# Kernel optimization log

Measured on AMD Instinct MI355X. Metric: run time of the kernel, lower is better.

The kernel has to match this reference:

```python
import jax, jax.numpy as jnp
import numpy as np


def _fracdiff(X, alpha):
    """Fractional differencing (1-L)^alpha applied per batch/channel.
    X: (B, T, n), alpha: (B, n) >= 0. Weights w_0 = 1, w_k = w_{k-1}*(k-1-alpha)/k.
    Y[b, t, i] = sum_{k=0..t} w[b, k, i] * X[b, t-k, i]  (causal filter).
    Computed as a linear convolution via FFT (same math, O(T log T)).
    """
    B, T, n = X.shape
    k = jnp.arange(1, T, dtype=X.dtype)[None, :, None]          # (1, T-1, 1)
    factors = (k - 1.0 - alpha[:, None, :]) / k                  # (B, T-1, n)
    w = jnp.concatenate(
        [jnp.ones((B, 1, n), X.dtype), jnp.cumprod(factors, axis=1)], axis=1
    )                                                            # (B, T, n)
    L = 2 * T  # zero-pad to avoid circular wrap-around
    Xf = jnp.fft.rfft(X, n=L, axis=1)
    Wf = jnp.fft.rfft(w, n=L, axis=1)
    Y = jnp.fft.irfft(Xf * Wf, n=L, axis=1)[:, :T, :]
    return Y.astype(X.dtype)


def setup_inputs() -> dict:
    key = jax.random.key(0)
    kx, ka, kA = jax.random.split(key, 3)
    B, T, n = 8, 8192, 128
    X = jax.random.normal(kx, (B, T, n), dtype=jnp.float32)
    # normalize per trial/channel, mirroring normalize_data=True in __init__
    X = (X - X.mean(axis=1, keepdims=True)) / X.std(axis=1, keepdims=True, ddof=1)
    alpha = jax.random.uniform(ka, (B, n), dtype=jnp.float32)
    A = jax.random.normal(kA, (B, n, n), dtype=jnp.float32) * 0.1
    return {"X": X, "alpha": alpha, "A": A}


def reference(X, alpha, A):
    # _resid(): Y = fracdiff(X, relu(alpha)); E = Y[:,1:,:] - X[:,:-1,:] @ A^T
    Y = _fracdiff(X, jax.nn.relu(alpha))
    Yhat = jnp.einsum('bti,bji->btj', X[:, :-1, :], A)  # bmm(X, A.transpose(1,2))
    return Y[:, 1:, :] - Yhat
```

## Files before the change

### kernel.cpp

```cpp
#include <hip/hip_runtime.h>

#define T 8192
#define NCH 128
#define NB 8
#define NS (NB * NCH)
#define TM1 (T - 1)

typedef __bf16 v8bf __attribute__((ext_vector_type(8)));
typedef float v16f __attribute__((ext_vector_type(16)));

#define WREV_LEN 8448
#define WREV_COPY_STRIDE ((size_t)NS * WREV_LEN)

#define ILIM_TRUNC 144
#define KCHUNKS 19
#define WR_D_MIN 2880

struct __attribute__((packed, aligned(4))) U16 { uint4 v; };
struct __attribute__((packed, aligned(4))) F16V { float4 v; };

__device__ __forceinline__ uint bf_bits(float f) {
  union { float f; uint u; } v; v.f = f;
  return (v.u + 0x7FFFu + ((v.u >> 16) & 1u)) >> 16;
}

__device__ __forceinline__ uint wbits(const float* wsh, int k) {
  if ((unsigned)k > 8191u) return 0u;
  return bf_bits(wsh[k + (k >> 5)]);
}

__global__ __launch_bounds__(256) void wkern(const float* __restrict__ alpha,
                                             ushort* __restrict__ wr2) {
  const int sid = blockIdx.x;
  const float a = fmaxf(alpha[sid], 0.f);
  const int j = threadIdx.x;
  __shared__ float sc[256];
  __shared__ float wsh[8448];
  const int k0 = j << 5;
  float c = 1.f;
  #pragma unroll
  for (int s = 1; s <= 32; ++s) {
    const float k = (float)(k0 + s);
    c *= (k - 1.f - a) / k;
  }
  sc[j] = c;
  __syncthreads();
  for (int off = 1; off < 256; off <<= 1) {
    const float u = (j >= off) ? sc[j - off] : 1.f;
    const float v = sc[j];
    __syncthreads();
    sc[j] = u * v;
    __syncthreads();
  }
  float p = (j == 0) ? 1.f : sc[j - 1];
  wsh[k0 + j] = p;
  for (int s = 1; s < 32; ++s) {
    const float k = (float)(k0 + s);
    p *= (k - 1.f - a) / k;
    wsh[k0 + s + j] = p;
  }
  __syncthreads();
  uint* c0u = (uint*)(wr2 + (size_t)sid * WREV_LEN);
  uint* c1u = (uint*)(wr2 + WREV_COPY_STRIDE + (size_t)sid * WREV_LEN);
  for (int d = WR_D_MIN + j; d < WREV_LEN / 2; d += 256) {
    const int z = 2 * d;
    const uint a0 = wbits(wsh, 8319 - z);
    const uint a1 = wbits(wsh, 8318 - z);
    const uint a2 = wbits(wsh, 8317 - z);
    c0u[d] = a0 | (a1 << 16);
    c1u[d] = a1 | (a2 << 16);
  }
}

__global__ __launch_bounds__(256) void tkern(const float* __restrict__ X,
                                             ushort* __restrict__ xT) {
  __shared__ float tile[32][33];
  const int b = blockIdx.z;
  const int i0 = blockIdx.y << 5;
  const int t0 = blockIdx.x << 5;
  const int tx = threadIdx.x;
  const int ty = threadIdx.y;
  #pragma unroll
  for (int k = 0; k < 4; ++k) {
    const int t = t0 + ty + (k << 3);
    tile[ty + (k << 3)][tx] = X[((size_t)b * T + t) * NCH + i0 + tx];
  }
  __syncthreads();
  #pragma unroll
  for (int k = 0; k < 4; ++k) {
    const int i = i0 + ty + (k << 3);
    xT[((size_t)(b * NCH + i)) * T + t0 + tx] =
        (ushort)bf_bits(tile[tx][ty + (k << 3)]);
  }
}

__global__ __launch_bounds__(256, 2) void convk(const ushort* __restrict__ wr2,
                                                const ushort* __restrict__ xT,
                                                float* __restrict__ yT) {
  const int sid = blockIdx.x;
  const int tid = threadIdx.x;
  const int wave = tid >> 6;
  const int lane = tid & 63;
  const int ln31 = lane & 31;
  const int q = lane >> 5;

  __shared__ uint4 arena16[1280];

  {
    const int u = tid;
    arena16[((u & 7) * 160) + (u >> 3)] = make_uint4(0, 0, 0, 0);
  }
  {
    const uint4* xg16 = (const uint4*)(xT + (size_t)sid * T);
    for (int u0 = tid; u0 < 1024; u0 += 256) {
      const int u = u0 + 256;
      arena16[((u & 7) * 160) + (u >> 3)] = xg16[u0];
    }
  }
  __syncthreads();

  v16f acc[4][2];
  #pragma unroll
  for (int cc = 0; cc < 4; ++cc)
    #pragma unroll
    for (int rt = 0; rt < 2; ++rt)
      #pragma unroll
      for (int e = 0; e < 16; ++e) acc[cc][rt][e] = 0.f;

  const int s0_par = (8303 - ln31 + 8 * q) & 1;
  const uint* wu = (const uint*)(wr2 + (s0_par ? WREV_COPY_STRIDE : 0) +
                                 (size_t)sid * WREV_LEN);

  uint4 av[10];
  int dw0;
  {
    const int ibase0 = -4 + wave * 8;
    const int s0 = 8303 - 16 * ibase0 - ln31 + 8 * q;
    dw0 = (s0 - s0_par) >> 1;
    #pragma unroll
    for (int j2 = 0; j2 < 10; ++j2)
      av[j2] = ((const U16*)(wu + (dw0 - 8 * j2)))->v;
  }

  for (int K = wave; K < KCHUNKS; K += 4) {
    const int ibase = -4 + K * 8;
    const int dw0n = dw0 - 256;
    const bool more = (K + 4) < KCHUNKS;
    uint4 pf0, pf1, pf2, pf3;
    if (more) {
      pf0 = ((const U16*)(wu + dw0n))->v;
      pf1 = ((const U16*)(wu + (dw0n - 8)))->v;
      pf2 = ((const U16*)(wu + (dw0n - 16)))->v;
      pf3 = ((const U16*)(wu + (dw0n - 24)))->v;
    }
    #pragma unroll
    for (int ii = 0; ii < 8; ++ii) {
      const int i = ibase + ii;
      const v8bf A0 = __builtin_bit_cast(v8bf, av[ii]);
      const v8bf A1 = __builtin_bit_cast(v8bf, av[ii + 2]);
      const int m2 = -2 * (i + 1);
      const int u70 = m2 & 7;
      const int u71 = (m2 + 1) & 7;
      const int G0 = u70 * 160 + 32 + ((m2 - u70) >> 3);
      const int G1 = u71 * 160 + 32 + ((m2 + 1 - u71) >> 3);
      const int phi = ln31 + (q ? G1 : G0);
      #pragma unroll
      for (int cc = 0; cc < 4; ++cc) {
        if (i < (cc == 0 ? 128 : ILIM_TRUNC)) {
          const uint4 bv = arena16[phi + 32 * cc];
          const v8bf Bf = __builtin_bit_cast(v8bf, bv);
          acc[cc][0] = __builtin_amdgcn_mfma_f32_32x32x16_bf16(A0, Bf, acc[cc][0], 0, 0, 0);
          acc[cc][1] = __builtin_amdgcn_mfma_f32_32x32x16_bf16(A1, Bf, acc[cc][1], 0, 0, 0);
        }
      }
    }
    if (more) {
      av[0] = pf0; av[1] = pf1; av[2] = pf2; av[3] = pf3;
      #pragma unroll
      for (int j2 = 4; j2 < 10; ++j2)
        av[j2] = ((const U16*)(wu + (dw0n - 8 * j2)))->v;
    }
    dw0 = dw0n;
  }

  float* const zbase = (float*)arena16;
  const int rowq = 4 * q;
  #pragma unroll
  for (int cc = 0; cc < 4; ++cc) {
    #pragma unroll
    for (int rt = 0; rt < 2; ++rt) {
      __syncthreads();
      float* zone = zbase + wave * 1152;
      #pragma unroll
      for (int g = 0; g < 4; ++g) {
        float4 v = make_float4(acc[cc][rt][4 * g], acc[cc][rt][4 * g + 1],
                               acc[cc][rt][4 * g + 2], acc[cc][rt][4 * g + 3]);
        *(float4*)(zone + ln31 * 36 + 8 * g + rowq) = v;
      }
      __syncthreads();
      const int n2 = tid & 31, rg = tid >> 5;
      const int zi = n2 * 36 + 4 * rg;
      float4 s0 = *(const float4*)(zbase + 0 * 1152 + zi);
      float4 s1 = *(const float4*)(zbase + 1 * 1152 + zi);
      float4 s2 = *(const float4*)(zbase + 2 * 1152 + zi);
      float4 s3 = *(const float4*)(zbase + 3 * 1152 + zi);
      float4 s;
      s.x = s0.x + s1.x + s2.x + s3.x;
      s.y = s0.y + s1.y + s2.y + s3.y;
      s.z = s0.z + s1.z + s2.z + s3.z;
      s.w = s0.w + s1.w + s2.w + s3.w;
      *(float4*)(yT + (size_t)sid * T + 2048 * cc + 64 * n2 + 32 * rt + 4 * rg) = s;
    }
  }
}

__global__ __launch_bounds__(256) void outk(const float* __restrict__ X,
                                            const float* __restrict__ A,
                                            const float* __restrict__ yT,
                                            float* __restrict__ out) {
  const int b = blockIdx.y;
  const int t0 = blockIdx.x << 6;
  const int tid = threadIdx.x;
  const int wave = tid >> 6;
  const int lane = tid & 63;
  const int ln31 = lane & 31;
  const int q = lane >> 5;

  __shared__ uint4 arena[3072];

  {
    const float* Ab = A + (size_t)b * NCH * NCH;
    #pragma unroll
    for (int g = 0; g < 8; ++g) {
      const int u = g * 256 + tid;
      const int jr = u >> 4, c4 = u & 15;
      const float4 f0 = *(const float4*)(Ab + jr * NCH + 8 * c4);
      const float4 f1 = *(const float4*)(Ab + jr * NCH + 8 * c4 + 4);
      uint4 pk;
      pk.x = bf_bits(f0.x) | (bf_bits(f0.y) << 16);
      pk.y = bf_bits(f0.z) | (bf_bits(f0.w) << 16);
      pk.z = bf_bits(f1.x) | (bf_bits(f1.y) << 16);
      pk.w = bf_bits(f1.z) | (bf_bits(f1.w) << 16);
      arena[c4 * 128 + ((jr + c4) & 127)] = pk;
    }
  }
  {
    const float* Xb = X + ((size_t)b * T + t0) * NCH;
    #pragma unroll
    for (int g = 0; g < 4; ++g) {
      const int u = g * 256 + tid;
      const int m = u >> 4, c4 = u & 15;
      const float4 f0 = *(const float4*)(Xb + m * NCH + 8 * c4);
      const float4 f1 = *(const float4*)(Xb + m * NCH + 8 * c4 + 4);
      uint4 pk;
      pk.x = bf_bits(f0.x) | (bf_bits(f0.y) << 16);
      pk.y = bf_bits(f0.z) | (bf_bits(f0.w) << 16);
      pk.z = bf_bits(f1.x) | (bf_bits(f1.y) << 16);
      pk.w = bf_bits(f1.z) | (bf_bits(f1.w) << 16);
      arena[2048 + c4 * 64 + ((m + c4) & 63)] = pk;
    }
  }
  __syncthreads();

  v16f acc[2];
  #pragma unroll
  for (int mt = 0; mt < 2; ++mt)
    #pragma unroll
    for (int e = 0; e < 16; ++e) acc[mt][e] = 0.f;

  const int nt = wave;
  #pragma unroll
  for (int kk = 0; kk < 8; ++kk) {
    const int c4 = 2 * kk + q;
    const uint4 bv = arena[c4 * 128 + ((nt * 32 + ln31 + c4) & 127)];
    const v8bf Bf = __builtin_bit_cast(v8bf, bv);
    #pragma unroll
    for (int mt = 0; mt < 2; ++mt) {
      const uint4 avv = arena[2048 + c4 * 64 + ((mt * 32 + ln31 + c4) & 63)];
      const v8bf Af = __builtin_bit_cast(v8bf, avv);
      acc[mt] = __builtin_amdgcn_mfma_f32_32x32x16_bf16(Af, Bf, acc[mt], 0, 0, 0);
    }
  }

  const int jj = nt * 32 + ln31;
  const float* yg = yT + ((size_t)(b * NCH + jj)) * T;
  float* og = out + (size_t)b * TM1 * NCH + jj;
  #pragma unroll
  for (int mt = 0; mt < 2; ++mt) {
    #pragma unroll
    for (int g = 0; g < 4; ++g) {
      const int r0 = mt * 32 + 8 * g + 4 * q;
      const float4 yv = ((const F16V*)(yg + t0 + r0 + 1))->v;
      #pragma unroll
      for (int e = 0; e < 4; ++e) {
        const int t = t0 + r0 + e;
        const float val = ((const float*)&yv)[e] - acc[mt][4 * g + e];
        if (t < TM1) og[(size_t)t * NCH] = val;
      }
    }
  }
}

extern "C" void kernel_launch(void* const* d_in, const int* in_sizes, int n_in,
                              void* d_out, int out_size, void* d_ws, size_t ws_size,
                              hipStream_t stream) {
  const float* X     = (const float*)d_in[0];
  const float* alpha = (const float*)d_in[1];
  const float* A     = (const float*)d_in[2];
  float* out = (float*)d_out;
  char* ws = (char*)d_ws;

  ushort* wr2 = (ushort*)ws;
  ushort* xT  = (ushort*)(ws + 34603008);
  float*  yT  = (float*)(ws + 34603008 + 16777216);

  hipLaunchKernelGGL(wkern, dim3(NS), dim3(256), 0, stream, alpha, wr2);
  hipLaunchKernelGGL(tkern, dim3(T / 32, NCH / 32, NB), dim3(32, 8), 0, stream, X, xT);
  hipLaunchKernelGGL(convk, dim3(NS), dim3(256), 0, stream, wr2, xT, yT);
  hipLaunchKernelGGL(outk, dim3(T / 64, NB), dim3(256), 0, stream, X, A, yT, out);
}
```

Measured before the change: 156.6 us.

## Truncate weight generation to needed range and stage Y tile through LDS

The weight kernel now computes only the first 2560 fractional-difference weights (10 per thread instead of 32) with a padded LDS index, since the stored reversed weights only reference that range. The final epilogue first loads the Y tile into shared memory with coalesced row reads and then reads it transposed, replacing per-lane strided float4 global reads. This adds a barrier and LDS traffic. It relies on the assumption that weights beyond index 2559 are never needed.

```diff
diff --git a/kernel.cpp b/kernel.cpp
--- a/kernel.cpp
+++ b/kernel.cpp
@@ -15,6 +15,8 @@
 #define ILIM_TRUNC 144
 #define KCHUNKS 19
 #define WR_D_MIN 2880
+#define KMAX_W 2559
+#define NW 2560
 
 struct __attribute__((packed, aligned(4))) U16 { uint4 v; };
 struct __attribute__((packed, aligned(4))) F16V { float4 v; };
@@ -25,7 +27,7 @@
 }
 
 __device__ __forceinline__ uint wbits(const float* wsh, int k) {
-  if ((unsigned)k > 8191u) return 0u;
+  if ((unsigned)k > (unsigned)KMAX_W) return 0u;
   return bf_bits(wsh[k + (k >> 5)]);
 }
 
@@ -35,11 +37,11 @@
   const float a = fmaxf(alpha[sid], 0.f);
   const int j = threadIdx.x;
   __shared__ float sc[256];
-  __shared__ float wsh[8448];
-  const int k0 = j << 5;
+  __shared__ float wsh[NW + NW / 32];
+  const int k0 = j * 10;
   float c = 1.f;
   #pragma unroll
-  for (int s = 1; s <= 32; ++s) {
+  for (int s = 1; s <= 10; ++s) {
     const float k = (float)(k0 + s);
     c *= (k - 1.f - a) / k;
   }
@@ -53,11 +55,13 @@
     __syncthreads();
   }
   float p = (j == 0) ? 1.f : sc[j - 1];
-  wsh[k0 + j] = p;
-  for (int s = 1; s < 32; ++s) {
+  wsh[k0 + (k0 >> 5)] = p;
+  #pragma unroll
+  for (int s = 1; s < 10; ++s) {
     const float k = (float)(k0 + s);
     p *= (k - 1.f - a) / k;
-    wsh[k0 + s + j] = p;
+    const int kk = k0 + s;
+    wsh[kk + (kk >> 5)] = p;
   }
   __syncthreads();
   uint* c0u = (uint*)(wr2 + (size_t)sid * WREV_LEN);
@@ -282,19 +286,34 @@
     }
   }
 
+  __syncthreads();
+  float* const ldsY = (float*)arena;
+  {
+    const int jr = tid >> 1, h = tid & 1;
+    const float* yr = yT + ((size_t)(b * NCH + jr)) * T + t0 + 1 + 32 * h;
+    #pragma unroll
+    for (int v = 0; v < 8; ++v) {
+      const float4 f = ((const F16V*)(yr + 4 * v))->v;
+      const int tt = 32 * h + 4 * v;
+      ldsY[(tt + 0) * 132 + jr] = f.x;
+      ldsY[(tt + 1) * 132 + jr] = f.y;
+      ldsY[(tt + 2) * 132 + jr] = f.z;
+      ldsY[(tt + 3) * 132 + jr] = f.w;
+    }
+  }
+  __syncthreads();
+
   const int jj = nt * 32 + ln31;
-  const float* yg = yT + ((size_t)(b * NCH + jj)) * T;
   float* og = out + (size_t)b * TM1 * NCH + jj;
   #pragma unroll
   for (int mt = 0; mt < 2; ++mt) {
     #pragma unroll
     for (int g = 0; g < 4; ++g) {
       const int r0 = mt * 32 + 8 * g + 4 * q;
-      const float4 yv = ((const F16V*)(yg + t0 + r0 + 1))->v;
       #pragma unroll
       for (int e = 0; e < 4; ++e) {
         const int t = t0 + r0 + e;
-        const float val = ((const float*)&yv)[e] - acc[mt][4 * g + e];
+        const float val = ldsY[(r0 + e) * 132 + jj] - acc[mt][4 * g + e];
         if (t < TM1) og[(size_t)t * NCH] = val;
       }
     }
```

Result: faster. 148.9 us (-4.9%).
